# Performance work log

Measured on AMD Instinct MI355X. Metric: run time of the kernel, lower is better.

Reference implementation:

```python
import jax, jax.numpy as jnp
import numpy as np

LOW_T, HIGH_T = 100.0, 200.0  # cv2.Canny thresholds from source


def _conv3(x, k):
    # x: [B,H,W], k: [3,3]; replicate border like OpenCV BORDER_REPLICATE
    xp = jnp.pad(x, ((0, 0), (1, 1), (1, 1)), mode='edge')
    return jax.lax.conv_general_dilated(
        xp[:, None], k[None, None].astype(x.dtype),
        window_strides=(1, 1), padding='VALID')[:, 0]


def _shift(a, dy, dx):
    # zero-padded spatial shift: result[y,x] = a[y+dy, x+dx]
    B, H, W = a.shape
    ap = jnp.pad(a, ((0, 0), (1, 1), (1, 1)))
    return ap[:, 1 + dy:1 + dy + H, 1 + dx:1 + dx + W]


def canny(labels):
    # (labels*255).astype(uint8) quantization, kept as float
    img = jnp.floor(jnp.clip(labels, 0.0, 1.0) * 255.0)
    kx = jnp.array([[-1., 0., 1.], [-2., 0., 2.], [-1., 0., 1.]], img.dtype)
    ky = jnp.array([[-1., -2., -1.], [0., 0., 0.], [1., 2., 1.]], img.dtype)
    gx = _conv3(img, kx)
    gy = _conv3(img, ky)
    mag = jnp.abs(gx) + jnp.abs(gy)  # OpenCV default L1 gradient
    theta = jnp.mod(jnp.degrees(jnp.arctan2(gy, gx)), 180.0)
    b0 = (theta < 22.5) | (theta >= 157.5)
    b45 = (theta >= 22.5) & (theta < 67.5)
    b90 = (theta >= 67.5) & (theta < 112.5)
    # neighbors along gradient direction (non-maximum suppression)
    n1 = jnp.where(b0, _shift(mag, 0, 1),
         jnp.where(b45, _shift(mag, -1, 1),
         jnp.where(b90, _shift(mag, 1, 0), _shift(mag, -1, -1))))
    n2 = jnp.where(b0, _shift(mag, 0, -1),
         jnp.where(b45, _shift(mag, 1, -1),
         jnp.where(b90, _shift(mag, -1, 0), _shift(mag, 1, 1))))
    nms = (mag >= n1) & (mag >= n2)
    strong = nms & (mag > HIGH_T)
    weak = nms & (mag > LOW_T)

    def dilate(e):
        return jax.lax.reduce_window(e.astype(jnp.float32), 0.0, jax.lax.max,
                                     (1, 3, 3), (1, 1, 1), 'SAME') > 0

    # hysteresis: grow strong edges through weak pixels to fixpoint
    def body(state):
        e, _ = state
        ne = weak & dilate(e)
        return ne, jnp.any(ne != e)

    edges, _ = jax.lax.while_loop(lambda s: s[1], body, (strong, jnp.array(True)))
    return edges.astype(jnp.int32)  # binary {0,1} edge mask


def setup_inputs() -> dict:
    key = jax.random.key(0)
    k1, k2 = jax.random.split(key)
    pred = jax.random.normal(k1, (32, 2, 512, 512), dtype=jnp.float32)
    labels = jax.random.uniform(k2, (32, 512, 512), dtype=jnp.float32)
    return {"pred": pred, "labels": labels}


def reference(pred, labels):
    edge_mask = canny(labels)  # [B,H,W] int in {0,1}
    logp = jax.nn.log_softmax(pred, axis=1)  # [B,2,H,W]
    nll = -jnp.take_along_axis(logp, edge_mask[:, None], axis=1)[:, 0]
    return nll.mean()
```

## Files before the change

### kernel.cpp

```cpp
#include <hip/hip_runtime.h>

typedef unsigned long long u64;
typedef unsigned int u32;
typedef unsigned char u8;

#define IMH 512
#define IMW 512
#define NB 32
#define WPI 4096
#define NWORDS (NB*WPI)

#define QZ(v) floorf(fminf(fmaxf((v),0.f),1.f)*255.f)

#define LOADRAW(Y, V, HL, HR) do { \
    int _yc = (Y); _yc = _yc < 0 ? 0 : (_yc > 511 ? 511 : _yc); \
    const float* _row = img + _yc*IMW; \
    V = *(const float4*)&_row[xb]; \
    if (L0)  HL = *(const float2*)&_row[strip ? (X0-2) : 0]; \
    if (L63) HR = *(const float2*)&_row[strip ? 510 : (X0+256)]; \
} while(0)

#define NMSJ(J, QAm, QA0, QAp, PBm, PB0, PBp, CCm, CC0, CCp) do { \
    float m = PB0; \
    float gx_ = gxP[J], gy_ = gyP[J]; \
    float ax = fabsf(gx_), ay = fabsf(gy_); \
    bool c0_ = ay <  T1f*ax; \
    bool c90 = ay >= T2f*ax; \
    bool c45 = (!c0_) && (!c90) && (gx_*gy_ > 0.f); \
    float n1 = c0_ ? PBp : (c45 ? QAp : (c90 ? CC0 : QAm)); \
    float n2 = c0_ ? PBm : (c45 ? CCm : (c90 ? QA0 : CCp)); \
    if (m >= n1 && m >= n2) { \
        if (m > 100.f) wb |= (1u<<(J)); \
        if (m > 200.f) sb |= (1u<<(J)); \
    } \
} while(0)

#define STEP(Y, VIN, HLIN, HRIN, VNX, HLNX, HRNX, DOLOAD) do { \
    if (DOLOAD) LOADRAW((Y)+1, VNX, HLNX, HRNX); \
    float c0=QZ(VIN.x), c1=QZ(VIN.y), c2=QZ(VIN.z), c3=QZ(VIN.w); \
    float chl0 = QZ(HLIN.x), chl1 = strip ? QZ(HLIN.y) : QZ(HLIN.x); \
    float chr0 = strip ? QZ(HRIN.y) : QZ(HRIN.x), chr1 = QZ(HRIN.y); \
    float qn0=rP[0]+c0, qn1=rP[1]+c1, qn2=rP[2]+c2, qn3=rP[3]+c3; \
    float ql0=hPl0+chl0, ql1=hPl1+chl1, qr0=hPr0+chr0, qr1=hPr1+chr1; \
    float t1_0=qP[0]+qn0, t1_1=qP[1]+qn1, t1_2=qP[2]+qn2, t1_3=qP[3]+qn3; \
    float t2_0=qn0-qP[0], t2_1=qn1-qP[1], t2_2=qn2-qP[2], t2_3=qn3-qP[3]; \
    float t1l0=qPl0+ql0, t2l0=ql0-qPl0, t1l1=qPl1+ql1, t2l1=ql1-qPl1; \
    float t1r0=qPr0+qr0, t2r0=qr0-qPr0, t1r1=qPr1+qr1, t2r1=qr1-qPr1; \
    float su1=__shfl_up(t1_3,1), su2=__shfl_up(t2_3,1); \
    float sd1=__shfl_down(t1_0,1), sd2=__shfl_down(t2_0,1); \
    float t1m = L0 ? t1l1 : su1, t2m = L0 ? t2l1 : su2; \
    float t1p = L63 ? t1r0 : sd1, t2p = L63 ? t2r0 : sd2; \
    const int ry = (Y)-1; \
    const bool rok = (ry >= 0) && (ry <= 511); \
    float gxc0 = t1_1-t1m,  gyc0 = t2m +2.f*t2_0+t2_1; \
    float gxc1 = t1_2-t1_0, gyc1 = t2_0+2.f*t2_1+t2_2; \
    float gxc2 = t1_3-t1_1, gyc2 = t2_1+2.f*t2_2+t2_3; \
    float gxc3 = t1p -t1_2, gyc3 = t2_2+2.f*t2_3+t2p; \
    float mc0 = rok ? fabsf(gxc0)+fabsf(gyc0) : 0.f; \
    float mc1 = rok ? fabsf(gxc1)+fabsf(gyc1) : 0.f; \
    float mc2 = rok ? fabsf(gxc2)+fabsf(gyc2) : 0.f; \
    float mc3 = rok ? fabsf(gxc3)+fabsf(gyc3) : 0.f; \
    float gxl = t1_0-t1l0, gyl = t2l0+2.f*t2l1+t2_0; \
    float gxr = t1r1-t1_3, gyr = t2_3+2.f*t2r0+t2r1; \
    float mlh = (rok && strip!=0) ? fabsf(gxl)+fabsf(gyl) : 0.f; \
    float mrh = (rok && strip!=1) ? fabsf(gxr)+fabsf(gyr) : 0.f; \
    float sum_ = __shfl_up(mc3,1), sdm_ = __shfl_down(mc0,1); \
    float mCL = L0 ? mlh : sum_; \
    float mCR = L63 ? mrh : sdm_; \
    if ((Y) >= y0+2) { \
        u32 sb=0, wb=0; \
        NMSJ(0, mgQL,  mgQ[0], mgQ[1], mgPL,  mgP[0], mgP[1], mCL, mc0, mc1); \
        NMSJ(1, mgQ[0],mgQ[1], mgQ[2], mgP[0],mgP[1], mgP[2], mc0, mc1, mc2); \
        NMSJ(2, mgQ[1],mgQ[2], mgQ[3], mgP[1],mgP[2], mgP[3], mc1, mc2, mc3); \
        NMSJ(3, mgQ[2],mgQ[3], mgQR,   mgP[2],mgP[3], mgPR,   mc2, mc3, mCR); \
        u32 pk = sb | (wb<<8); \
        u32 oth = __shfl_xor(pk, 1); \
        if (!(lane & 1)) { \
            size_t bix = ((size_t)(bimg*IMH + ((Y)-2)))*64 + strip*32 + (lane>>1); \
            edgeb[bix] = (u8)((sb & 0xFu) | ((oth & 0xFu) << 4)); \
            weakb[bix] = (u8)(((pk>>8) & 0xFu) | (((oth>>8) & 0xFu) << 4)); \
        } \
    } \
    mgQ[0]=mgP[0]; mgQ[1]=mgP[1]; mgQ[2]=mgP[2]; mgQ[3]=mgP[3]; \
    mgQL=mgPL; mgQR=mgPR; \
    mgP[0]=mc0; mgP[1]=mc1; mgP[2]=mc2; mgP[3]=mc3; \
    mgPL=mCL; mgPR=mCR; \
    gxP[0]=gxc0; gxP[1]=gxc1; gxP[2]=gxc2; gxP[3]=gxc3; \
    gyP[0]=gyc0; gyP[1]=gyc1; gyP[2]=gyc2; gyP[3]=gyc3; \
    qP[0]=qn0; qP[1]=qn1; qP[2]=qn2; qP[3]=qn3; \
    qPl0=ql0; qPl1=ql1; qPr0=qr0; qPr1=qr1; \
    rP[0]=c0; rP[1]=c1; rP[2]=c2; rP[3]=c3; \
    hPl0=chl0; hPl1=chl1; hPr0=chr0; hPr1=chr1; \
} while(0)

__global__ __launch_bounds__(64) void k_sobel_nms(
    const float* __restrict__ labels,
    u8* __restrict__ edgeb,
    u8* __restrict__ weakb)
{
    const int lane  = threadIdx.x;
    const int bx    = blockIdx.x;
    const int bimg  = bx >> 7;
    const int strip = bx & 1;
    const int band  = (bx >> 1) & 63;
    const int X0 = strip*256;
    const int y0 = band*8;
    const int xb = X0 + 4*lane;
    const bool L0 = (lane==0), L63 = (lane==63);
    const float* img = labels + (size_t)bimg*(IMH*IMW);
    const float T1f = 0.41421356237309503f;
    const float T2f = 2.4142135623730951f;

    float rP[4];
    float hPl0,hPl1,hPr0,hPr1;
    float qP[4];
    float qPl0,qPl1,qPr0,qPr1;
    float mgQ[4], mgP[4];
    float mgQL,mgQR,mgPL,mgPR;
    float gxP[4], gyP[4];

    float4 vA, vB;
    float2 hlA = make_float2(0.f,0.f), hlB = make_float2(0.f,0.f);
    float2 hrA = make_float2(0.f,0.f), hrB = make_float2(0.f,0.f);

    LOADRAW(y0-2, vA, hlA, hrA);
    LOADRAW(y0-1, vB, hlB, hrB);
    {
        float a0=QZ(vA.x), a1=QZ(vA.y), a2=QZ(vA.z), a3=QZ(vA.w);
        float b0=QZ(vB.x), b1=QZ(vB.y), b2=QZ(vB.z), b3=QZ(vB.w);
        qP[0]=a0+b0; qP[1]=a1+b1; qP[2]=a2+b2; qP[3]=a3+b3;
        rP[0]=b0; rP[1]=b1; rP[2]=b2; rP[3]=b3;
        float al0 = QZ(hlA.x), al1 = strip ? QZ(hlA.y) : QZ(hlA.x);
        float ar0 = strip ? QZ(hrA.y) : QZ(hrA.x), ar1 = QZ(hrA.y);
        hPl0 = QZ(hlB.x); hPl1 = strip ? QZ(hlB.y) : QZ(hlB.x);
        hPr0 = strip ? QZ(hrB.y) : QZ(hrB.x); hPr1 = QZ(hrB.y);
        qPl0 = al0 + hPl0; qPl1 = al1 + hPl1;
        qPr0 = ar0 + hPr0; qPr1 = ar1 + hPr1;
    }
#pragma unroll
    for (int j=0;j<4;++j) { mgQ[j]=0.f; mgP[j]=0.f; gxP[j]=0.f; gyP[j]=0.f; }
    mgQL=mgQR=mgPL=mgPR=0.f;

    LOADRAW(y0, vA, hlA, hrA);

#pragma unroll 1
    for (int y = y0; y < y0+10; y += 2) {
        STEP(y,   vA, hlA, hrA, vB, hlB, hrB, (y+1 <= y0+9));
        STEP(y+1, vB, hlB, hrB, vA, hlA, hrA, (y+2 <= y0+9));
    }
}

#define H2ROWS 64
#define H2HALO 32
#define H2LDSR 128

__device__ inline u64 hz3(u64 l, u64 c, u64 r) {
    return c | (c<<1) | (c>>1) | (l>>63) | (r<<63);
}

__global__ __launch_bounds__(256) void k_hyst1(
    u64* __restrict__ edgew,
    const u64* __restrict__ weakw)
{
    __shared__ u64 ed[H2LDSR][9];
    __shared__ u64 wk[H2LDSR][9];
    __shared__ int s_chg;
    const int tid = threadIdx.x;
    const int strip = blockIdx.x & 7, b = blockIdx.x >> 3;
    const int y0 = strip*H2ROWS;
    u64* eb = edgew + (size_t)b*WPI;
    const u64* wb = weakw + (size_t)b*WPI;

#pragma unroll
    for (int k = 0; k < 4; ++k) {
        int w = tid + k*256;
        int r = w >> 3, c = w & 7;
        int gr = y0 - H2HALO + r;
        u64 e = 0, ww = 0;
        if (gr >= 0 && gr < IMH) { e = eb[gr*8+c]; ww = wb[gr*8+c]; }
        ed[r][c] = e; wk[r][c] = ww;
    }
    const int c  = tid & 7;
    const int r0 = 4*(tid >> 3);
    __syncthreads();

    for (int iter = 0; iter < 32; ++iter) {
        if (tid == 0) s_chg = 0;
        __syncthreads();
        u64 H[6];
#pragma unroll
        for (int j = 0; j < 6; ++j) {
            int r = r0 - 1 + j;
            u64 lm = 0, cc = 0, rr = 0;
            if (r >= 0 && r < H2LDSR) {
                cc = ed[r][c];
                lm = (c > 0) ? ed[r][c-1] : 0;
                rr = (c < 7) ? ed[r][c+1] : 0;
            }
            H[j] = hz3(lm, cc, rr);
        }
        bool chg = false;
#pragma unroll
        for (int i = 0; i < 4; ++i) {
            u64 old = ed[r0+i][c];
            u64 nw  = wk[r0+i][c] & (H[i] | H[i+1] | H[i+2]);
            if (nw != old) { ed[r0+i][c] = nw; chg = true; }
        }
        if (chg) s_chg = 1;
        __syncthreads();
        if (s_chg == 0) break;
    }

#pragma unroll
    for (int i = 0; i < 4; ++i) {
        int r = r0 + i;
        if (r >= H2HALO && r < H2HALO + H2ROWS)
            eb[(y0 - H2HALO + r)*8 + c] = ed[r][c];
    }
}

__global__ __launch_bounds__(256) void k_loss(
    const float* __restrict__ pred,
    const u64* __restrict__ edgew,
    double* __restrict__ partial)
{
    const int t = blockIdx.x*256 + threadIdx.x;
    float4 P0[4], P1[4];
    u64 W[4];
#pragma unroll
    for (int k = 0; k < 4; ++k) {
        int g = t + k*524288;
        int b = g >> 16, rem4 = g & 65535;
        P0[k] = *(const float4*)&pred[((size_t)(2*b)  <<18) + 4*(size_t)rem4];
        P1[k] = *(const float4*)&pred[((size_t)(2*b+1)<<18) + 4*(size_t)rem4];
        W[k]  = edgew[(b<<12) | (rem4>>4)];
    }
    float acc[4];
#pragma unroll
    for (int k = 0; k < 4; ++k) {
        int g = t + k*524288;
        int rem4 = g & 65535;
        u32 nib = (u32)(W[k] >> ((rem4 & 15)*4)) & 0xFu;
        float d0=P1[k].x-P0[k].x, d1=P1[k].y-P0[k].y;
        float d2=P1[k].z-P0[k].z, d3=P1[k].w-P0[k].w;
        float t0_ = (nib&1u) ? -d0 : d0;
        float t1_ = (nib&2u) ? -d1 : d1;
        float t2_ = (nib&4u) ? -d2 : d2;
        float t3_ = (nib&8u) ? -d3 : d3;
        float s0 = fmaxf(t0_,0.f) + __logf(1.f + __expf(-fabsf(t0_)));
        float s1 = fmaxf(t1_,0.f) + __logf(1.f + __expf(-fabsf(t1_)));
        float s2 = fmaxf(t2_,0.f) + __logf(1.f + __expf(-fabsf(t2_)));
        float s3 = fmaxf(t3_,0.f) + __logf(1.f + __expf(-fabsf(t3_)));
        acc[k] = (s0+s1)+(s2+s3);
    }
    double s = ((double)acc[0]+(double)acc[1]) + ((double)acc[2]+(double)acc[3]);
#pragma unroll
    for (int off = 32; off > 0; off >>= 1) s += __shfl_down(s, off);
    __shared__ double sh[4];
    if ((threadIdx.x & 63) == 0) sh[threadIdx.x>>6] = s;
    __syncthreads();
    if (threadIdx.x == 0) partial[blockIdx.x] = (sh[0]+sh[1])+(sh[2]+sh[3]);
}

__global__ __launch_bounds__(256) void k_final(
    const double* __restrict__ partial, float* __restrict__ out)
{
    double s = 0.0;
    for (int i = threadIdx.x; i < 2048; i += 256) s += partial[i];
#pragma unroll
    for (int off = 32; off > 0; off >>= 1) s += __shfl_down(s, off);
    __shared__ double sh[4];
    if ((threadIdx.x & 63) == 0) sh[threadIdx.x>>6] = s;
    __syncthreads();
    if (threadIdx.x == 0)
        out[0] = (float)(((sh[0]+sh[1])+(sh[2]+sh[3])) * (1.0/8388608.0));
}

extern "C" void kernel_launch(void* const* d_in, const int* in_sizes, int n_in,
                              void* d_out, int out_size, void* d_ws, size_t ws_size,
                              hipStream_t stream)
{
    const float* pred   = (const float*)d_in[0];
    const float* labels = (const float*)d_in[1];
    float* out = (float*)d_out;

    char* ws = (char*)d_ws;
    double* partial = (double*)ws;
    u64*    edgew   = (u64*)(ws + 32768);
    u64*    weakw   = edgew + NWORDS;

    k_sobel_nms<<<4096, 64, 0, stream>>>(labels, (u8*)edgew, (u8*)weakw);
    k_hyst1<<<256, 256, 0, stream>>>(edgew, weakw);
    k_loss<<<2048, 256, 0, stream>>>(pred, edgew, partial);
    k_final<<<1, 256, 0, stream>>>(partial, out);
}
```

Measured before the change: 50.65 us.

## Overlap loss with sobel in one launch and apply edge correction in hysteresis

Merges the loss pass and the Sobel/NMS pass into one heterogeneous launch. Loss blocks compute softplus(d) over all pixels as if no pixel were an edge, while separate blocks run the Sobel waves. Hysteresis then subtracts d for the edge pixels, reading either a packed fp16 copy of d or pred directly, and writes that correction into extra partial slots. This removes one kernel launch and the separate edge-mask readback, and lets the pred streaming overlap the image processing. In exchange, the fp16 rounding of d adds a small accuracy risk and the d buffer adds write traffic.

```diff
diff --git a/kernel.cpp b/kernel.cpp
--- a/kernel.cpp
+++ b/kernel.cpp
@@ -1,4 +1,5 @@
 #include <hip/hip_runtime.h>
+#include <hip/hip_fp16.h>
 
 typedef unsigned long long u64;
 typedef unsigned int u32;
@@ -93,16 +94,15 @@
     hPl0=chl0; hPl1=chl1; hPr0=chr0; hPr1=chr1; \
 } while(0)
 
-__global__ __launch_bounds__(64) void k_sobel_nms(
+__device__ __forceinline__ void sobel_wave(
     const float* __restrict__ labels,
     u8* __restrict__ edgeb,
-    u8* __restrict__ weakb)
-{
-    const int lane  = threadIdx.x;
-    const int bx    = blockIdx.x;
-    const int bimg  = bx >> 7;
-    const int strip = bx & 1;
-    const int band  = (bx >> 1) & 63;
+    u8* __restrict__ weakb,
+    int vbx, int lane)
+{
+    const int bimg  = vbx >> 7;
+    const int strip = vbx & 1;
+    const int band  = (vbx >> 1) & 63;
     const int X0 = strip*256;
     const int y0 = band*8;
     const int xb = X0 + 4*lane;
@@ -150,6 +150,63 @@
     }
 }
 
+__global__ __launch_bounds__(256) void k_front(
+    const float* __restrict__ pred,
+    const float* __restrict__ labels,
+    u8* __restrict__ edgeb,
+    u8* __restrict__ weakb,
+    u32* __restrict__ dpack,
+    double* __restrict__ partial,
+    int store_d)
+{
+    if (blockIdx.x < 2048) {
+        const int t = blockIdx.x*256 + threadIdx.x;
+        float4 P0[4], P1[4];
+#pragma unroll
+        for (int k = 0; k < 4; ++k) {
+            int g = t + k*524288;
+            int b = g >> 16, rem4 = g & 65535;
+            P0[k] = *(const float4*)&pred[((size_t)(2*b)  <<18) + 4*(size_t)rem4];
+            P1[k] = *(const float4*)&pred[((size_t)(2*b+1)<<18) + 4*(size_t)rem4];
+        }
+        __builtin_amdgcn_sched_barrier(0);
+        float acc[4];
+        uint2 st[4];
+#pragma unroll
+        for (int k = 0; k < 4; ++k) {
+            float d0=P1[k].x-P0[k].x, d1=P1[k].y-P0[k].y;
+            float d2=P1[k].z-P0[k].z, d3=P1[k].w-P0[k].w;
+            float s0 = fmaxf(d0,0.f) + __logf(1.f + __expf(-fabsf(d0)));
+            float s1 = fmaxf(d1,0.f) + __logf(1.f + __expf(-fabsf(d1)));
+            float s2 = fmaxf(d2,0.f) + __logf(1.f + __expf(-fabsf(d2)));
+            float s3 = fmaxf(d3,0.f) + __logf(1.f + __expf(-fabsf(d3)));
+            acc[k] = (s0+s1)+(s2+s3);
+            __half2 h01 = __floats2half2_rn(d0,d1);
+            __half2 h23 = __floats2half2_rn(d2,d3);
+            st[k].x = *(u32*)&h01;
+            st[k].y = *(u32*)&h23;
+        }
+        if (store_d) {
+#pragma unroll
+            for (int k = 0; k < 4; ++k) {
+                int g = t + k*524288;
+                ((uint2*)dpack)[g] = st[k];
+            }
+        }
+        double s = ((double)acc[0]+(double)acc[1]) + ((double)acc[2]+(double)acc[3]);
+#pragma unroll
+        for (int off = 32; off > 0; off >>= 1) s += __shfl_down(s, off);
+        __shared__ double sh[4];
+        if ((threadIdx.x & 63) == 0) sh[threadIdx.x>>6] = s;
+        __syncthreads();
+        if (threadIdx.x == 0) partial[blockIdx.x] = (sh[0]+sh[1])+(sh[2]+sh[3]);
+    } else {
+        sobel_wave(labels, edgeb, weakb,
+                   (blockIdx.x - 2048)*4 + (threadIdx.x >> 6),
+                   threadIdx.x & 63);
+    }
+}
+
 #define H2ROWS 64
 #define H2HALO 32
 #define H2LDSR 128
@@ -158,9 +215,13 @@
     return c | (c<<1) | (c>>1) | (l>>63) | (r<<63);
 }
 
-__global__ __launch_bounds__(256) void k_hyst1(
-    u64* __restrict__ edgew,
-    const u64* __restrict__ weakw)
+template<int MODE>
+__global__ __launch_bounds__(256) void k_hyst(
+    const u64* __restrict__ edgew,
+    const u64* __restrict__ weakw,
+    const u32* __restrict__ dpack,
+    const float* __restrict__ pred,
+    double* __restrict__ partial)
 {
     __shared__ u64 ed[H2LDSR][9];
     __shared__ u64 wk[H2LDSR][9];
@@ -168,7 +229,7 @@
     const int tid = threadIdx.x;
     const int strip = blockIdx.x & 7, b = blockIdx.x >> 3;
     const int y0 = strip*H2ROWS;
-    u64* eb = edgew + (size_t)b*WPI;
+    const u64* eb = edgew + (size_t)b*WPI;
     const u64* wb = weakw + (size_t)b*WPI;
 
 #pragma unroll
@@ -211,66 +272,49 @@
         if (s_chg == 0) break;
     }
 
-#pragma unroll
-    for (int i = 0; i < 4; ++i) {
-        int r = r0 + i;
-        if (r >= H2HALO && r < H2HALO + H2ROWS)
-            eb[(y0 - H2HALO + r)*8 + c] = ed[r][c];
-    }
-}
-
-__global__ __launch_bounds__(256) void k_loss(
-    const float* __restrict__ pred,
-    const u64* __restrict__ edgew,
-    double* __restrict__ partial)
-{
-    const int t = blockIdx.x*256 + threadIdx.x;
-    float4 P0[4], P1[4];
-    u64 W[4];
-#pragma unroll
-    for (int k = 0; k < 4; ++k) {
-        int g = t + k*524288;
-        int b = g >> 16, rem4 = g & 65535;
-        P0[k] = *(const float4*)&pred[((size_t)(2*b)  <<18) + 4*(size_t)rem4];
-        P1[k] = *(const float4*)&pred[((size_t)(2*b+1)<<18) + 4*(size_t)rem4];
-        W[k]  = edgew[(b<<12) | (rem4>>4)];
-    }
-    float acc[4];
-#pragma unroll
-    for (int k = 0; k < 4; ++k) {
-        int g = t + k*524288;
-        int rem4 = g & 65535;
-        u32 nib = (u32)(W[k] >> ((rem4 & 15)*4)) & 0xFu;
-        float d0=P1[k].x-P0[k].x, d1=P1[k].y-P0[k].y;
-        float d2=P1[k].z-P0[k].z, d3=P1[k].w-P0[k].w;
-        float t0_ = (nib&1u) ? -d0 : d0;
-        float t1_ = (nib&2u) ? -d1 : d1;
-        float t2_ = (nib&4u) ? -d2 : d2;
-        float t3_ = (nib&8u) ? -d3 : d3;
-        float s0 = fmaxf(t0_,0.f) + __logf(1.f + __expf(-fabsf(t0_)));
-        float s1 = fmaxf(t1_,0.f) + __logf(1.f + __expf(-fabsf(t1_)));
-        float s2 = fmaxf(t2_,0.f) + __logf(1.f + __expf(-fabsf(t2_)));
-        float s3 = fmaxf(t3_,0.f) + __logf(1.f + __expf(-fabsf(t3_)));
-        acc[k] = (s0+s1)+(s2+s3);
-    }
-    double s = ((double)acc[0]+(double)acc[1]) + ((double)acc[2]+(double)acc[3]);
-#pragma unroll
-    for (int off = 32; off > 0; off >>= 1) s += __shfl_down(s, off);
-    __shared__ double sh[4];
-    if ((threadIdx.x & 63) == 0) sh[threadIdx.x>>6] = s;
+    const int c8 = tid >> 5;
+    const u32 s2 = (u32)((2*tid) & 63);
+    double es = 0.0;
+    if (MODE) {
+        const u32* dp = dpack + (((size_t)b*IMH + y0) << 8);
+#pragma unroll 8
+        for (int r = 0; r < 64; ++r) {
+            u32 pk = dp[(r<<8) + tid];
+            u64 w = ed[H2HALO + r][c8];
+            float2 f = __half22float2(*(__half2*)&pk);
+            if ((w >> s2) & 1)     es += (double)f.x;
+            if ((w >> (s2+1)) & 1) es += (double)f.y;
+        }
+    } else {
+        const float* pb0 = pred + (((size_t)(2*b))<<18) + (size_t)y0*IMW;
+        const float* pb1 = pb0 + (1<<18);
+#pragma unroll 4
+        for (int r = 0; r < 64; ++r) {
+            float2 a0 = *(const float2*)&pb0[r*IMW + 2*tid];
+            float2 a1 = *(const float2*)&pb1[r*IMW + 2*tid];
+            u64 w = ed[H2HALO + r][c8];
+            if ((w >> s2) & 1)     es += (double)(a1.x - a0.x);
+            if ((w >> (s2+1)) & 1) es += (double)(a1.y - a0.y);
+        }
+    }
+#pragma unroll
+    for (int off = 32; off > 0; off >>= 1) es += __shfl_down(es, off);
+    __shared__ double shq[4];
+    if ((tid & 63) == 0) shq[tid>>6] = es;
     __syncthreads();
-    if (threadIdx.x == 0) partial[blockIdx.x] = (sh[0]+sh[1])+(sh[2]+sh[3]);
-}
-
-__global__ __launch_bounds__(256) void k_final(
+    if (tid == 0) partial[2048 + blockIdx.x] = (shq[0]+shq[1])+(shq[2]+shq[3]);
+}
+
+__global__ __launch_bounds__(256) void k_final2(
     const double* __restrict__ partial, float* __restrict__ out)
 {
     double s = 0.0;
     for (int i = threadIdx.x; i < 2048; i += 256) s += partial[i];
-#pragma unroll
-    for (int off = 32; off > 0; off >>= 1) s += __shfl_down(s, off);
+    double v = s - partial[2048 + threadIdx.x];
+#pragma unroll
+    for (int off = 32; off > 0; off >>= 1) v += __shfl_down(v, off);
     __shared__ double sh[4];
-    if ((threadIdx.x & 63) == 0) sh[threadIdx.x>>6] = s;
+    if ((threadIdx.x & 63) == 0) sh[threadIdx.x>>6] = v;
     __syncthreads();
     if (threadIdx.x == 0)
         out[0] = (float)(((sh[0]+sh[1])+(sh[2]+sh[3])) * (1.0/8388608.0));
@@ -288,9 +332,15 @@
     double* partial = (double*)ws;
     u64*    edgew   = (u64*)(ws + 32768);
     u64*    weakw   = edgew + NWORDS;
-
-    k_sobel_nms<<<4096, 64, 0, stream>>>(labels, (u8*)edgew, (u8*)weakw);
-    k_hyst1<<<256, 256, 0, stream>>>(edgew, weakw);
-    k_loss<<<2048, 256, 0, stream>>>(pred, edgew, partial);
-    k_final<<<1, 256, 0, stream>>>(partial, out);
-}
+    u32*    dpack   = (u32*)(ws + 32768 + 2*(size_t)NWORDS*8);
+    const size_t need = 32768 + 2*(size_t)NWORDS*8 + (size_t)4194304*4;
+    const int use_dpack = (ws_size >= need) ? 1 : 0;
+
+    k_front<<<3072, 256, 0, stream>>>(pred, labels, (u8*)edgew, (u8*)weakw,
+                                      dpack, partial, use_dpack);
+    if (use_dpack)
+        k_hyst<1><<<256, 256, 0, stream>>>(edgew, weakw, dpack, pred, partial);
+    else
+        k_hyst<0><<<256, 256, 0, stream>>>(edgew, weakw, dpack, pred, partial);
+    k_final2<<<1, 256, 0, stream>>>(partial, out);
+}
```

Measured after the change: 47.16 us. 1.07x faster.
